# Optimization experiments

Hardware: AMD Instinct MI355X
Metric: run time of the kernel (lower is better)

Reference implementation:

```python
import jax, jax.numpy as jnp
import numpy as np

D = 1024      # input_dim / embed_dim
H = 1024      # hidden_dim
H2 = H // 2
M = 15        # n_masks
NH = 4        # n_heads
B = 8192
LN_EPS = 1e-5


def setup_inputs() -> dict:
    key = jax.random.key(0)
    ks = jax.random.split(key, 16)
    s = 0.02
    return {
        "x": jax.random.normal(ks[0], (B, D), jnp.float32),
        # nn.MultiheadAttention params (torch layout: y = x @ W.T + b)
        "in_proj_w": jax.random.normal(ks[1], (3 * D, D), jnp.float32) * s,
        "in_proj_b": jax.random.normal(ks[2], (3 * D,), jnp.float32) * s,
        "out_proj_w": jax.random.normal(ks[3], (D, D), jnp.float32) * s,
        "out_proj_b": jax.random.normal(ks[4], (D,), jnp.float32) * s,
        # 15 mask MLPs stacked along leading axis (grouped GEMM form)
        "W1": jax.random.normal(ks[5], (M, D, H), jnp.float32) * s,
        "b1": jax.random.normal(ks[6], (M, H), jnp.float32) * s,
        "ln_g": jnp.ones((M, H), jnp.float32),
        "ln_b": jnp.zeros((M, H), jnp.float32),
        "W2": jax.random.normal(ks[7], (M, H, H2), jnp.float32) * s,
        "b2": jax.random.normal(ks[8], (M, H2), jnp.float32) * s,
        "W3": jax.random.normal(ks[9], (M, H2, D), jnp.float32) * s,
        "b3": jax.random.normal(ks[10], (M, D), jnp.float32) * s,
    }


def reference(x, in_proj_w, in_proj_b, out_proj_w, out_proj_b,
              W1, b1, ln_g, ln_b, W2, b2, W3, b3):
    Bn = x.shape[0]
    hd = D // NH
    # --- seq_len=1 self-attention ---
    qkv = x @ in_proj_w.T + in_proj_b                      # [B, 3D]
    q, k, v = jnp.split(qkv, 3, axis=-1)                   # each [B, D]
    qh = q.reshape(Bn, NH, hd)
    kh = k.reshape(Bn, NH, hd)
    vh = v.reshape(Bn, NH, hd)
    scores = jnp.sum(qh * kh, axis=-1) / jnp.sqrt(jnp.float32(hd))  # [B, NH]
    # softmax over kv length = 1 -> all ones (kept for faithfulness)
    w = jax.nn.softmax(scores[..., None], axis=-1)         # [B, NH, 1]
    attn = (w * vh).reshape(Bn, D)                         # [B, D]
    a = attn @ out_proj_w.T + out_proj_b                   # [B, D]
    # --- 15 mask MLPs as one grouped GEMM stack (Dropout is eval->identity) ---
    h1 = jnp.einsum('bd,mdh->mbh', a, W1) + b1[:, None, :]  # [M, B, H]
    mu = jnp.mean(h1, axis=-1, keepdims=True)
    var = jnp.mean(jnp.square(h1 - mu), axis=-1, keepdims=True)
    h1 = (h1 - mu) * jax.lax.rsqrt(var + LN_EPS) * ln_g[:, None, :] + ln_b[:, None, :]
    h1 = jax.nn.gelu(h1, approximate=False)
    h2 = jnp.einsum('mbh,mhk->mbk', h1, W2) + b2[:, None, :]  # [M, B, H2]
    h2 = jax.nn.gelu(h2, approximate=False)
    h3 = jnp.einsum('mbk,mkd->mbd', h2, W3) + b3[:, None, :]  # [M, B, D]
    return jax.nn.sigmoid(h3)                               # [M, B, D]
```

## Files before the change

### kernel.cpp

```cpp
#include <hip/hip_runtime.h>

#define D_  1024
#define H_  1024
#define H2_ 512
#define M_  15
#define B_  8192

typedef __attribute__((ext_vector_type(4))) float f32x4;
typedef __attribute__((ext_vector_type(8))) short short8;

__device__ __forceinline__ unsigned short f2bf(float f) {
  unsigned int u = __float_as_uint(f);
  u += 0x7fffu + ((u >> 16) & 1u);
  return (unsigned short)(u >> 16);
}
__device__ __forceinline__ float bf2f(unsigned int h) {
  return __uint_as_float(h << 16);
}
__device__ __forceinline__ float gelu_exact(float x) {
  return 0.5f * x * (1.0f + erff(x * 0.70710678118654752440f));
}

__global__ void cast_f32_bf16(const float* __restrict__ in, unsigned short* __restrict__ out, int n4) {
  int i = blockIdx.x * blockDim.x + threadIdx.x;
  if (i >= n4) return;
  float4 v = ((const float4*)in)[i];
  ushort4 o;
  o.x = f2bf(v.x); o.y = f2bf(v.y); o.z = f2bf(v.z); o.w = f2bf(v.w);
  ((ushort4*)out)[i] = o;
}

__global__ void transpose_cast(const float* __restrict__ in, unsigned short* __restrict__ out,
                               int K, int N) {
  __shared__ float t[32][33];
  const size_t mo = (size_t)blockIdx.z * K * N;
  in  += mo;
  out += mo;
  const int k0 = blockIdx.x * 32, n0 = blockIdx.y * 32;
  const int tx = threadIdx.x, ty = threadIdx.y;
#pragma unroll
  for (int j = 0; j < 32; j += 8)
    t[ty + j][tx] = in[(size_t)(k0 + ty + j) * N + (n0 + tx)];
  __syncthreads();
#pragma unroll
  for (int j = 0; j < 32; j += 8)
    out[(size_t)(n0 + ty + j) * K + (k0 + tx)] = f2bf(t[tx][ty + j]);
}

template <int EPI>
__launch_bounds__(256, 3)
__global__ void gemm_bt(const unsigned short* __restrict__ A, const unsigned short* __restrict__ Bt,
                        const float* __restrict__ bias, void* __restrict__ Cout,
                        int Mrows, int N, int K,
                        long sA, long sB, long sBias, long sC) {
  __shared__ __align__(16) unsigned short As[128 * 64];
  __shared__ __align__(16) unsigned short Bs[128 * 64];
  const int mz = blockIdx.z;
  A    += (size_t)mz * sA;
  Bt   += (size_t)mz * sB;
  bias += (size_t)mz * sBias;

  const int tid  = threadIdx.x;
  const int w    = tid >> 6;
  const int lane = tid & 63;
  const int row0 = blockIdx.x * 128;
  const int col0 = blockIdx.y * 128;

  f32x4 acc[4][4];
#pragma unroll
  for (int i = 0; i < 4; ++i)
#pragma unroll
    for (int j = 0; j < 4; ++j) acc[i][j] = (f32x4){0.f, 0.f, 0.f, 0.f};

  const int wm = w >> 1, wn = w & 1;
  const int mrow = lane & 15;
  const int kq   = (lane >> 4) << 3;

  for (int k0 = 0; k0 < K; k0 += 64) {
    __syncthreads();
#pragma unroll
    for (int i = 0; i < 4; ++i) {
      const int c  = i * 256 + tid;
      const int m  = c >> 3;
      const int kk = (c & 7) << 3;
      const unsigned short* gA = A  + (size_t)(row0 + m) * K + (k0 + kk);
      const unsigned short* gB = Bt + (size_t)(col0 + m) * K + (k0 + kk);
      const int ldsoff = (i * 256 + w * 64) * 8;
      __builtin_amdgcn_global_load_lds((const __attribute__((address_space(1))) void*)gA,
                                       (__attribute__((address_space(3))) void*)(As + ldsoff),
                                       16, 0, 0);
      __builtin_amdgcn_global_load_lds((const __attribute__((address_space(1))) void*)gB,
                                       (__attribute__((address_space(3))) void*)(Bs + ldsoff),
                                       16, 0, 0);
    }
    __syncthreads();
#pragma unroll
    for (int ki = 0; ki < 64; ki += 32) {
      short8 af[4], bf[4];
#pragma unroll
      for (int f = 0; f < 4; ++f) {
        af[f] = *(const short8*)(As + (wm * 64 + f * 16 + mrow) * 64 + ki + kq);
        bf[f] = *(const short8*)(Bs + (wn * 64 + f * 16 + mrow) * 64 + ki + kq);
      }
#pragma unroll
      for (int fm = 0; fm < 4; ++fm)
#pragma unroll
        for (int fn = 0; fn < 4; ++fn)
          acc[fm][fn] = __builtin_amdgcn_mfma_f32_16x16x32_bf16(af[fm], bf[fn], acc[fm][fn], 0, 0, 0);
    }
  }

  float*          Cf = (float*)Cout          + (size_t)mz * sC;
  unsigned short* Cb = (unsigned short*)Cout + (size_t)mz * sC;
  const int rq = (lane >> 4) << 2;
  const int cl = lane & 15;
#pragma unroll
  for (int fm = 0; fm < 4; ++fm) {
#pragma unroll
    for (int fn = 0; fn < 4; ++fn) {
      const int cc = col0 + wn * 64 + fn * 16 + cl;
      const float bv = bias[cc];
#pragma unroll
      for (int r = 0; r < 4; ++r) {
        const int rr = row0 + wm * 64 + fm * 16 + rq + r;
        float v = acc[fm][fn][r] + bv;
        if (EPI == 2) {
          Cf[(size_t)rr * N + cc] = 1.0f / (1.0f + __expf(-v));
        } else {
          if (EPI == 1) v = gelu_exact(v);
          Cb[(size_t)rr * N + cc] = f2bf(v);
        }
      }
    }
  }
}

#define BAR()   asm volatile("s_barrier" ::: "memory")
#define LGKM0() asm volatile("s_waitcnt lgkmcnt(0)" ::: "memory")
#define VM6()   asm volatile("s_waitcnt vmcnt(6)" ::: "memory")

#define STG_A(bufi, bA, rho0) do {                                                             \
  _Pragma("unroll")                                                                            \
  for (int j_ = 0; j_ < 2; ++j_) {                                                             \
    const int rho_ = (rho0) + j_ * 64 + (tid >> 3);                                            \
    const int gr_  = (((rho_ >> 6) & 1) << 7) | (((rho_ >> 7) & 1) << 6) | (rho_ & 63);        \
    const unsigned short* g_ = (bA) + (size_t)gr_ * K + (((tid & 7) ^ (rho_ & 7)) << 3);       \
    __builtin_amdgcn_global_load_lds((const __attribute__((address_space(1))) void*)g_,        \
        (__attribute__((address_space(3))) void*)(&As[bufi][(rho0) * 64 + (j_ * 512 + w6 * 64) * 8]), \
        16, 0, 0);                                                                             \
  }                                                                                            \
} while (0)

#define STG_B(bufi, bB, rho0) do {                                                             \
  _Pragma("unroll")                                                                            \
  for (int j_ = 0; j_ < 2; ++j_) {                                                             \
    const int rho_ = (rho0) + j_ * 64 + (tid >> 3);                                            \
    const int gc_  = (((rho_ >> 5) & 3) << 6) | (((rho_ >> 7) & 1) << 5) | (rho_ & 31);        \
    const unsigned short* g_ = (bB) + (size_t)gc_ * K + (((tid & 7) ^ (rho_ & 7)) << 3);       \
    __builtin_amdgcn_global_load_lds((const __attribute__((address_space(1))) void*)g_,        \
        (__attribute__((address_space(3))) void*)(&Bs[bufi][(rho0) * 64 + (j_ * 512 + w6 * 64) * 8]), \
        16, 0, 0);                                                                             \
  }                                                                                            \
} while (0)

#define LDA4(bufi, hi) do {                                                                    \
  _Pragma("unroll")                                                                            \
  for (int q_ = 0; q_ < 4; ++q_) {                                                             \
    const int rho_ = ((hi) ? 128 : 0) + wm * 64 + q_ * 16 + lrow;                              \
    a[q_][0] = *(const short8*)&As[bufi][rho_ * 64 + ((lk ^ (rho_ & 7)) << 3)];                \
    a[q_][1] = *(const short8*)&As[bufi][rho_ * 64 + (((4 + lk) ^ (rho_ & 7)) << 3)];          \
  }                                                                                            \
} while (0)

#define LDB2(bufi, hi) do {                                                                    \
  _Pragma("unroll")                                                                            \
  for (int q_ = 0; q_ < 2; ++q_) {                                                             \
    const int rho_ = ((hi) ? 128 : 0) + wn * 32 + q_ * 16 + lrow;                              \
    b[(hi) * 2 + q_][0] = *(const short8*)&Bs[bufi][rho_ * 64 + ((lk ^ (rho_ & 7)) << 3)];     \
    b[(hi) * 2 + q_][1] = *(const short8*)&Bs[bufi][rho_ * 64 + (((4 + lk) ^ (rho_ & 7)) << 3)]; \
  }                                                                                            \
} while (0)

#define MMQ(mh, nh) do {                                                                       \
  __builtin_amdgcn_s_setprio(1);                                                               \
  _Pragma("unroll")                                                                            \
  for (int mq_ = 0; mq_ < 4; ++mq_) {                                                          \
    _Pragma("unroll")                                                                          \
    for (int nq_ = 0; nq_ < 2; ++nq_) {                                                        \
      acc[(mh) * 4 + mq_][(nh) * 2 + nq_] = __builtin_amdgcn_mfma_f32_16x16x32_bf16(           \
          a[mq_][0], b[(nh) * 2 + nq_][0], acc[(mh) * 4 + mq_][(nh) * 2 + nq_], 0, 0, 0);      \
      acc[(mh) * 4 + mq_][(nh) * 2 + nq_] = __builtin_amdgcn_mfma_f32_16x16x32_bf16(           \
          a[mq_][1], b[(nh) * 2 + nq_][1], acc[(mh) * 4 + mq_][(nh) * 2 + nq_], 0, 0, 0);      \
    }                                                                                          \
  }                                                                                            \
  __builtin_amdgcn_s_setprio(0);                                                               \
} while (0)

template <int EPI, int LNT, int LGY>
__launch_bounds__(512, 2)
__global__ void gemm256p(const unsigned short* __restrict__ A, const unsigned short* __restrict__ Bt,
                         const float* __restrict__ bias, void* __restrict__ Cout,
                         int N, int K, long sA, long sB, long sBias, long sC,
                         int ntiles8, int tpb) {
  __shared__ __align__(16) unsigned short As[2][256 * 64];
  __shared__ __align__(16) unsigned short Bs[2][256 * 64];
  const int NT = 1 << LNT, GYm1 = (1 << LGY) - 1;

  const int bid = blockIdx.x;
  const int xcd = bid & 7, lb = bid >> 3;
  const int cb  = xcd * ntiles8;

  const int tid  = threadIdx.x;
  const int w6   = tid >> 6;
  const int lane = tid & 63;
  const int wm   = w6 >> 2;
  const int wn   = w6 & 3;
  const int lrow = lane & 15;
  const int lk   = lane >> 4;

  int t_cur = 0;
  int tix  = cb + lb;
  int row0 = ((tix >> LGY) & 31) << 8;
  int col0 = (tix & GYm1) << 8;
  int mz   = tix >> (LGY + 5);
  const unsigned short* bAc = A  + (size_t)mz * sA + (size_t)row0 * K;
  const unsigned short* bBc = Bt + (size_t)mz * sB + (size_t)col0 * K;

  f32x4 acc[8][4];
#pragma unroll
  for (int i = 0; i < 8; ++i)
#pragma unroll
    for (int j = 0; j < 4; ++j) acc[i][j] = (f32x4){0.f, 0.f, 0.f, 0.f};
  short8 a[4][2], b[4][2];

  STG_A(0, bAc, 0); STG_B(0, bBc, 0); STG_B(0, bBc, 128); STG_A(0, bAc, 128);
  STG_A(1, bAc + 64, 0); STG_B(1, bBc + 64, 0); STG_B(1, bBc + 64, 128);
  VM6(); BAR();

  const int totK = tpb << LNT;
#pragma unroll 1
  for (int T = 0; T < totK; T += 2) {
    const int g2 = (T + 2 < totK) ? T + 2 : totK - 1;
    const int g3 = (T + 3 < totK) ? T + 3 : totK - 1;
    const int t2 = g2 >> LNT, t3 = g3 >> LNT;
    const int tix2 = cb + lb + t2 * 30;
    const int tix3 = cb + lb + t3 * 30;
    const unsigned short* bA2 = A  + (size_t)(tix2 >> (LGY + 5)) * sA
                                   + (size_t)((((tix2 >> LGY) & 31) << 8)) * K + ((g2 & (NT - 1)) << 6);
    const unsigned short* bB2 = Bt + (size_t)(tix2 >> (LGY + 5)) * sB
                                   + (size_t)(((tix2 & GYm1) << 8)) * K + ((g2 & (NT - 1)) << 6);
    const unsigned short* bA3 = A  + (size_t)(tix3 >> (LGY + 5)) * sA
                                   + (size_t)((((tix3 >> LGY) & 31) << 8)) * K + ((g3 & (NT - 1)) << 6);
    const unsigned short* bB3 = Bt + (size_t)(tix3 >> (LGY + 5)) * sB
                                   + (size_t)(((tix3 & GYm1) << 8)) * K + ((g3 & (NT - 1)) << 6);
    const unsigned short* bA1 = bAc + (((T + 1) & (NT - 1)) << 6);

    LDA4(0, 0); LDB2(0, 0);
    STG_A(1, bA1, 128);
    BAR(); LGKM0(); MMQ(0, 0); BAR();
    LDB2(0, 1);
    STG_A(0, bA2, 0);
    BAR(); LGKM0(); MMQ(0, 1); BAR();
    LDA4(0, 1);
    STG_B(0, bB2, 0);
    BAR(); LGKM0(); MMQ(1, 0); BAR();
    STG_B(0, bB2, 128);
    VM6(); BAR(); MMQ(1, 1); BAR();
    LDA4(1, 0); LDB2(1, 0);
    STG_A(0, bA2, 128);
    BAR(); LGKM0(); MMQ(0, 0); BAR();
    LDB2(1, 1);
    STG_A(1, bA3, 0);
    BAR(); LGKM0(); MMQ(0, 1); BAR();
    LDA4(1, 1);
    STG_B(1, bB3, 0);
    BAR(); LGKM0(); MMQ(1, 0); BAR();
    STG_B(1, bB3, 128);
    VM6(); BAR(); MMQ(1, 1); BAR();

    if (((T + 2) & (NT - 1)) == 0) {
      const float* bp = bias + (size_t)mz * sBias;
      float*          Cf = (float*)Cout          + (size_t)mz * sC;
      unsigned short* Cb = (unsigned short*)Cout + (size_t)mz * sC;
      const int rq = (lane >> 4) << 2;
      const int cl = lane & 15;
#pragma unroll
      for (int nf = 0; nf < 4; ++nf) {
        const int cc = col0 + wn * 64 + nf * 16 + cl;
        const float bv = bp[cc];
#pragma unroll
        for (int mf = 0; mf < 8; ++mf) {
#pragma unroll
          for (int r = 0; r < 4; ++r) {
            const int rr = row0 + wm * 128 + mf * 16 + rq + r;
            float v = acc[mf][nf][r] + bv;
            if (EPI == 2) {
              Cf[(size_t)rr * N + cc] = 1.0f / (1.0f + __expf(-v));
            } else {
              if (EPI == 1) v = gelu_exact(v);
              Cb[(size_t)rr * N + cc] = f2bf(v);
            }
          }
        }
      }
#pragma unroll
      for (int i = 0; i < 8; ++i)
#pragma unroll
        for (int j = 0; j < 4; ++j) acc[i][j] = (f32x4){0.f, 0.f, 0.f, 0.f};
      ++t_cur;
      if (t_cur < tpb) {
        tix  = cb + lb + t_cur * 30;
        row0 = ((tix >> LGY) & 31) << 8;
        col0 = (tix & GYm1) << 8;
        mz   = tix >> (LGY + 5);
        bAc  = A  + (size_t)mz * sA + (size_t)row0 * K;
        bBc  = Bt + (size_t)mz * sB + (size_t)col0 * K;
      }
    }
  }
  asm volatile("s_waitcnt vmcnt(0)" ::: "memory");
}

__global__ void ln_gelu(const unsigned short* __restrict__ in, const float* __restrict__ g,
                        const float* __restrict__ bb, unsigned short* __restrict__ out) {
  const int m = blockIdx.y;
  in  += (size_t)m * B_ * H_;
  out += (size_t)m * B_ * H_;
  g   += (size_t)m * H_;
  bb  += (size_t)m * H_;
  const int row = blockIdx.x;
  const int tid = threadIdx.x;
  const unsigned short* rp = in + (size_t)row * H_;
  uint2 u = ((const uint2*)rp)[tid];
  float x0 = bf2f(u.x & 0xffffu);
  float x1 = bf2f(u.x >> 16);
  float x2 = bf2f(u.y & 0xffffu);
  float x3 = bf2f(u.y >> 16);

  float s  = x0 + x1 + x2 + x3;
  float s2 = x0 * x0 + x1 * x1 + x2 * x2 + x3 * x3;
#pragma unroll
  for (int o = 32; o > 0; o >>= 1) {
    s  += __shfl_down(s, o);
    s2 += __shfl_down(s2, o);
  }
  __shared__ float red[10];
  const int w = tid >> 6;
  if ((tid & 63) == 0) { red[w] = s; red[4 + w] = s2; }
  __syncthreads();
  if (tid == 0) {
    float ts = red[0] + red[1] + red[2] + red[3];
    float t2 = red[4] + red[5] + red[6] + red[7];
    float mean = ts * (1.0f / H_);
    float var  = t2 * (1.0f / H_) - mean * mean;
    red[8] = mean;
    red[9] = rsqrtf(var + 1e-5f);
  }
  __syncthreads();
  const float mean = red[8], rstd = red[9];
  const int col = tid * 4;
  float y0 = gelu_exact((x0 - mean) * rstd * g[col + 0] + bb[col + 0]);
  float y1 = gelu_exact((x1 - mean) * rstd * g[col + 1] + bb[col + 1]);
  float y2 = gelu_exact((x2 - mean) * rstd * g[col + 2] + bb[col + 2]);
  float y3 = gelu_exact((x3 - mean) * rstd * g[col + 3] + bb[col + 3]);
  ushort4 o;
  o.x = f2bf(y0); o.y = f2bf(y1); o.z = f2bf(y2); o.w = f2bf(y3);
  ((ushort4*)(out + (size_t)row * H_))[tid] = o;
}

extern "C" void kernel_launch(void* const* d_in, const int* in_sizes, int n_in,
                              void* d_out, int out_size, void* d_ws, size_t ws_size,
                              hipStream_t stream) {
  const float* x   = (const float*)d_in[0];
  const float* ipw = (const float*)d_in[1];
  const float* ipb = (const float*)d_in[2];
  const float* opw = (const float*)d_in[3];
  const float* opb = (const float*)d_in[4];
  const float* W1  = (const float*)d_in[5];
  const float* b1  = (const float*)d_in[6];
  const float* lng = (const float*)d_in[7];
  const float* lnb = (const float*)d_in[8];
  const float* W2  = (const float*)d_in[9];
  const float* b2  = (const float*)d_in[10];
  const float* W3  = (const float*)d_in[11];
  const float* b3  = (const float*)d_in[12];
  float* out = (float*)d_out;

  char* p = (char*)d_ws;
  auto take = [&](size_t bytes) { void* q = (void*)p; p += (bytes + 255) & ~(size_t)255; return q; };
  unsigned short* xb  = (unsigned short*)take((size_t)B_ * D_ * 2);
  unsigned short* wvb = (unsigned short*)take((size_t)D_ * D_ * 2);
  unsigned short* wob = (unsigned short*)take((size_t)D_ * D_ * 2);
  unsigned short* w1t = (unsigned short*)take((size_t)M_ * H_ * D_ * 2);
  unsigned short* w2t = (unsigned short*)take((size_t)M_ * H2_ * H_ * 2);
  unsigned short* w3t = (unsigned short*)take((size_t)M_ * D_ * H2_ * 2);
  unsigned short* vb  = (unsigned short*)take((size_t)B_ * D_ * 2);
  unsigned short* ab  = (unsigned short*)take((size_t)B_ * D_ * 2);
  unsigned short* h1p = (unsigned short*)take((size_t)M_ * B_ * H_ * 2);
  unsigned short* h1a = (unsigned short*)take((size_t)M_ * B_ * H_ * 2);
  unsigned short* h2b = (unsigned short*)take((size_t)M_ * B_ * H2_ * 2);

  cast_f32_bf16<<<dim3((B_ * D_ / 4 + 255) / 256), 256, 0, stream>>>(x, xb, B_ * D_ / 4);
  cast_f32_bf16<<<dim3((D_ * D_ / 4 + 255) / 256), 256, 0, stream>>>(ipw + 2 * D_ * D_, wvb, D_ * D_ / 4);
  cast_f32_bf16<<<dim3((D_ * D_ / 4 + 255) / 256), 256, 0, stream>>>(opw, wob, D_ * D_ / 4);
  transpose_cast<<<dim3(D_ / 32, H_ / 32, M_), dim3(32, 8), 0, stream>>>(W1, w1t, D_, H_);
  transpose_cast<<<dim3(H_ / 32, H2_ / 32, M_), dim3(32, 8), 0, stream>>>(W2, w2t, H_, H2_);
  transpose_cast<<<dim3(H2_ / 32, D_ / 32, M_), dim3(32, 8), 0, stream>>>(W3, w3t, H2_, D_);

  gemm_bt<0><<<dim3(B_ / 128, D_ / 128, 1), 256, 0, stream>>>(
      xb, wvb, ipb + 2 * D_, vb, B_, D_, D_, 0, 0, 0, 0);
  gemm_bt<0><<<dim3(B_ / 128, D_ / 128, 1), 256, 0, stream>>>(
      vb, wob, opb, ab, B_, D_, D_, 0, 0, 0, 0);

  gemm256p<0, 4, 2><<<dim3(240), 512, 0, stream>>>(
      ab, w1t, b1, h1p, H_, D_,
      0, (long)H_ * D_, (long)H_, (long)B_ * H_, 1920 / 8, 8);
  ln_gelu<<<dim3(B_, M_), 256, 0, stream>>>(h1p, lng, lnb, h1a);
  gemm256p<1, 4, 1><<<dim3(240), 512, 0, stream>>>(
      h1a, w2t, b2, h2b, H2_, H_,
      (long)B_ * H_, (long)H2_ * H_, (long)H2_, (long)B_ * H2_, 960 / 8, 4);
  gemm256p<2, 3, 2><<<dim3(240), 512, 0, stream>>>(
      h2b, w3t, b3, out, D_, H2_,
      (long)B_ * H2_, (long)D_ * H2_, (long)D_, (long)B_ * D_, 1920 / 8, 8);
}
```

Baseline: 1.623 ms.

## Fold V and output projections into one combined weight; batch gemm256p pipeline stages

Since softmax over a length-1 sequence is all ones, the attention output equals the V projection. The two chained BxDxD GEMMs are therefore replaced by a small DxDxD GEMM computing Wo·Wv, a bias fold (Wo·bv + bo), and a single BxDxD GEMM. This removes one large GEMM and the intermediate vb buffer, but adds an extra bf16 rounding of the combined weight. The gemm256p main loop is also reordered to issue two MMQ quadrants per barrier pair, grouping LDS loads and global stages to halve the barrier count, which risks register and latency pressure.

```diff
diff --git a/kernel.cpp b/kernel.cpp
--- a/kernel.cpp
+++ b/kernel.cpp
@@ -28,6 +28,22 @@
   ushort4 o;
   o.x = f2bf(v.x); o.y = f2bf(v.y); o.z = f2bf(v.z); o.w = f2bf(v.w);
   ((ushort4*)out)[i] = o;
+}
+
+__global__ void zero_f32(float* __restrict__ p, int n) {
+  int i = blockIdx.x * blockDim.x + threadIdx.x;
+  if (i < n) p[i] = 0.f;
+}
+
+__global__ void bias_fold(const float* __restrict__ opw, const float* __restrict__ bv,
+                          const float* __restrict__ opb, float* __restrict__ bc) {
+  const int o = blockIdx.x;
+  const int l = threadIdx.x;
+  float s = 0.f;
+  for (int d = l; d < D_; d += 64) s += opw[(size_t)o * D_ + d] * bv[d];
+#pragma unroll
+  for (int off = 32; off > 0; off >>= 1) s += __shfl_down(s, off);
+  if (l == 0) bc[o] = s + opb[o];
 }
 
 __global__ void transpose_cast(const float* __restrict__ in, unsigned short* __restrict__ out,
@@ -255,28 +271,26 @@
                                    + (size_t)(((tix3 & GYm1) << 8)) * K + ((g3 & (NT - 1)) << 6);
     const unsigned short* bA1 = bAc + (((T + 1) & (NT - 1)) << 6);
 
-    LDA4(0, 0); LDB2(0, 0);
+    LDA4(0, 0); LDB2(0, 0); LDB2(0, 1);
     STG_A(1, bA1, 128);
-    BAR(); LGKM0(); MMQ(0, 0); BAR();
-    LDB2(0, 1);
-    STG_A(0, bA2, 0);
-    BAR(); LGKM0(); MMQ(0, 1); BAR();
+    BAR(); LGKM0();
+    MMQ(0, 0); MMQ(0, 1);
+    BAR();
     LDA4(0, 1);
-    STG_B(0, bB2, 0);
-    BAR(); LGKM0(); MMQ(1, 0); BAR();
-    STG_B(0, bB2, 128);
-    VM6(); BAR(); MMQ(1, 1); BAR();
-    LDA4(1, 0); LDB2(1, 0);
+    STG_A(0, bA2, 0); STG_B(0, bB2, 0); STG_B(0, bB2, 128);
+    VM6(); BAR(); LGKM0();
+    MMQ(1, 0); MMQ(1, 1);
+    BAR();
+    LDA4(1, 0); LDB2(1, 0); LDB2(1, 1);
     STG_A(0, bA2, 128);
-    BAR(); LGKM0(); MMQ(0, 0); BAR();
-    LDB2(1, 1);
-    STG_A(1, bA3, 0);
-    BAR(); LGKM0(); MMQ(0, 1); BAR();
+    BAR(); LGKM0();
+    MMQ(0, 0); MMQ(0, 1);
+    BAR();
     LDA4(1, 1);
-    STG_B(1, bB3, 0);
-    BAR(); LGKM0(); MMQ(1, 0); BAR();
-    STG_B(1, bB3, 128);
-    VM6(); BAR(); MMQ(1, 1); BAR();
+    STG_A(1, bA3, 0); STG_B(1, bB3, 0); STG_B(1, bB3, 128);
+    VM6(); BAR(); LGKM0();
+    MMQ(1, 0); MMQ(1, 1);
+    BAR();
 
     if (((T + 2) & (NT - 1)) == 0) {
       const float* bp = bias + (size_t)mz * sBias;
@@ -389,28 +403,32 @@
   char* p = (char*)d_ws;
   auto take = [&](size_t bytes) { void* q = (void*)p; p += (bytes + 255) & ~(size_t)255; return q; };
   unsigned short* xb  = (unsigned short*)take((size_t)B_ * D_ * 2);
-  unsigned short* wvb = (unsigned short*)take((size_t)D_ * D_ * 2);
   unsigned short* wob = (unsigned short*)take((size_t)D_ * D_ * 2);
+  unsigned short* wvt = (unsigned short*)take((size_t)D_ * D_ * 2);
+  unsigned short* wcb = (unsigned short*)take((size_t)D_ * D_ * 2);
+  float*          zb  = (float*)take((size_t)D_ * 4);
+  float*          bc  = (float*)take((size_t)D_ * 4);
   unsigned short* w1t = (unsigned short*)take((size_t)M_ * H_ * D_ * 2);
   unsigned short* w2t = (unsigned short*)take((size_t)M_ * H2_ * H_ * 2);
   unsigned short* w3t = (unsigned short*)take((size_t)M_ * D_ * H2_ * 2);
-  unsigned short* vb  = (unsigned short*)take((size_t)B_ * D_ * 2);
   unsigned short* ab  = (unsigned short*)take((size_t)B_ * D_ * 2);
   unsigned short* h1p = (unsigned short*)take((size_t)M_ * B_ * H_ * 2);
   unsigned short* h1a = (unsigned short*)take((size_t)M_ * B_ * H_ * 2);
   unsigned short* h2b = (unsigned short*)take((size_t)M_ * B_ * H2_ * 2);
 
   cast_f32_bf16<<<dim3((B_ * D_ / 4 + 255) / 256), 256, 0, stream>>>(x, xb, B_ * D_ / 4);
-  cast_f32_bf16<<<dim3((D_ * D_ / 4 + 255) / 256), 256, 0, stream>>>(ipw + 2 * D_ * D_, wvb, D_ * D_ / 4);
   cast_f32_bf16<<<dim3((D_ * D_ / 4 + 255) / 256), 256, 0, stream>>>(opw, wob, D_ * D_ / 4);
+  transpose_cast<<<dim3(D_ / 32, D_ / 32, 1), dim3(32, 8), 0, stream>>>(ipw + 2 * D_ * D_, wvt, D_, D_);
   transpose_cast<<<dim3(D_ / 32, H_ / 32, M_), dim3(32, 8), 0, stream>>>(W1, w1t, D_, H_);
   transpose_cast<<<dim3(H_ / 32, H2_ / 32, M_), dim3(32, 8), 0, stream>>>(W2, w2t, H_, H2_);
   transpose_cast<<<dim3(H2_ / 32, D_ / 32, M_), dim3(32, 8), 0, stream>>>(W3, w3t, H2_, D_);
-
+  zero_f32<<<dim3(4), 256, 0, stream>>>(zb, D_);
+
+  gemm_bt<0><<<dim3(D_ / 128, D_ / 128, 1), 256, 0, stream>>>(
+      wob, wvt, zb, wcb, D_, D_, D_, 0, 0, 0, 0);
+  bias_fold<<<dim3(D_), 64, 0, stream>>>(opw, ipb + 2 * D_, opb, bc);
   gemm_bt<0><<<dim3(B_ / 128, D_ / 128, 1), 256, 0, stream>>>(
-      xb, wvb, ipb + 2 * D_, vb, B_, D_, D_, 0, 0, 0, 0);
-  gemm_bt<0><<<dim3(B_ / 128, D_ / 128, 1), 256, 0, stream>>>(
-      vb, wob, opb, ab, B_, D_, D_, 0, 0, 0, 0);
+      xb, wcb, bc, ab, B_, D_, D_, 0, 0, 0, 0);
 
   gemm256p<0, 4, 2><<<dim3(240), 512, 0, stream>>>(
       ab, w1t, b1, h1p, H_, D_,
```

After: 1.666 ms. 1.03x slower.
